# Optimization experiments

Hardware: AMD Instinct MI355X
Metric: run time of the kernel (lower is better)

## Reference

```python
import jax, jax.numpy as jnp
import numpy as np

B, TD, ND, FD, H = 16384, 256, 256, 512, 8
HID = [512, 256]


def _ln(x, g, b, eps=1e-5):
    m = jnp.mean(x, -1, keepdims=True)
    v = jnp.mean((x - m) ** 2, -1, keepdims=True)
    return (x - m) * jax.lax.rsqrt(v + eps) * g + b


def _mha1(q_in, k_in, v_in, wq, bq, wk, bk, wv, bv, wo, bo):
    # MultiheadAttention with seq_len=1 on both sides; eval mode (dropout off).
    Bq, E = q_in.shape
    dh = E // H
    q = (q_in @ wq.T + bq).reshape(Bq, H, dh)
    k = (k_in @ wk.T + bk).reshape(Bq, H, dh)
    scores = jnp.sum(q * k, -1) / np.sqrt(dh)          # [B, H]
    w = jax.nn.softmax(scores[..., None], axis=-1)      # [B, H, 1] -> exactly 1 (single key)
    attn = jnp.mean(w, axis=1)[:, None, :]              # averaged over heads -> [B, 1, 1]
    v = v_in @ wv.T + bv                                # attn weight == 1, so attn_out == v
    out = v @ wo.T + bo
    return out, attn


def setup_inputs():
    key = jax.random.key(0)
    ks = iter(jax.random.split(key, 40))
    def p(*shape):
        return jax.random.normal(next(ks), shape, dtype=jnp.float32) * 0.02
    inp = {
        'text_emb': jax.random.normal(next(ks), (B, TD), dtype=jnp.float32),
        'num_emb': jax.random.normal(next(ks), (B, ND), dtype=jnp.float32),
        'tp_w': p(FD, TD), 'tp_b': p(FD),
        'np_w': p(FD, ND), 'np_b': p(FD),
        'a1_wq': p(FD, FD), 'a1_wk': p(FD, FD), 'a1_wv': p(FD, FD),
        'a1_bq': p(FD), 'a1_bk': p(FD), 'a1_bv': p(FD),
        'a1_wo': p(FD, FD), 'a1_bo': p(FD),
        'a2_wq': p(FD, FD), 'a2_wk': p(FD, FD), 'a2_wv': p(FD, FD),
        'a2_bq': p(FD), 'a2_bk': p(FD), 'a2_bv': p(FD),
        'a2_wo': p(FD, FD), 'a2_bo': p(FD),
        'n1_g': jnp.ones((FD,), jnp.float32), 'n1_b': jnp.zeros((FD,), jnp.float32),
        'n2_g': jnp.ones((FD,), jnp.float32), 'n2_b': jnp.zeros((FD,), jnp.float32),
        'g_w': p(FD, 2 * FD), 'g_b': p(FD),
        'm1_w': p(HID[0], 2 * FD), 'm1_b': p(HID[0]),
        'ln1_g': jnp.ones((HID[0],), jnp.float32), 'ln1_b': jnp.zeros((HID[0],), jnp.float32),
        'm2_w': p(HID[1], HID[0]), 'm2_b': p(HID[1]),
        'ln2_g': jnp.ones((HID[1],), jnp.float32), 'ln2_b': jnp.zeros((HID[1],), jnp.float32),
    }
    return inp


def reference(text_emb, num_emb, tp_w, tp_b, np_w, np_b,
              a1_wq, a1_wk, a1_wv, a1_bq, a1_bk, a1_bv, a1_wo, a1_bo,
              a2_wq, a2_wk, a2_wv, a2_bq, a2_bk, a2_bv, a2_wo, a2_bo,
              n1_g, n1_b, n2_g, n2_b, g_w, g_b,
              m1_w, m1_b, ln1_g, ln1_b, m2_w, m2_b, ln2_g, ln2_b):
    t = text_emb @ tp_w.T + tp_b                        # [B, FD]
    n = num_emb @ np_w.T + np_b                         # [B, FD]
    n2t, attn_n2t = _mha1(n, t, t, a1_wq, a1_bq, a1_wk, a1_bk, a1_wv, a1_bv, a1_wo, a1_bo)
    n2t = _ln(n + n2t, n1_g, n1_b)
    t2n, attn_t2n = _mha1(t, n, n, a2_wq, a2_bq, a2_wk, a2_bk, a2_wv, a2_bv, a2_wo, a2_bo)
    t2n = _ln(t + t2n, n2_g, n2_b)
    comb = jnp.concatenate([n2t, t2n], axis=-1)         # [B, 2*FD]
    gate = jax.nn.sigmoid(comb @ g_w.T + g_b)           # [B, FD]
    h = jax.nn.gelu(_ln(comb @ m1_w.T + m1_b, ln1_g, ln1_b), approximate=False)
    fused = jax.nn.gelu(_ln(h @ m2_w.T + m2_b, ln2_g, ln2_b), approximate=False)
    return fused, gate, attn_n2t, attn_t2n
```

## Files before the change

### kernel.cpp

```cpp
#include <hip/hip_runtime.h>
#include <math.h>

typedef unsigned short u16;
typedef __bf16 bf16x8 __attribute__((ext_vector_type(8)));
typedef float f32x4 __attribute__((ext_vector_type(4)));
typedef short s16x8 __attribute__((ext_vector_type(8)));
typedef short s16x4 __attribute__((ext_vector_type(4)));

__device__ __forceinline__ float b2f(u16 u) {
    union { unsigned i; float f; } c; c.i = ((unsigned)u) << 16; return c.f;
}
__device__ __forceinline__ u16 f2b(float f) {
    union { float f; unsigned i; } c; c.f = f;
    return (u16)((c.i + 0x7fffu + ((c.i >> 16) & 1u)) >> 16);
}
__device__ __forceinline__ float gelu_f(float v) {
    return 0.5f * v * (1.0f + erff(v * 0.70710678118654752f));
}
__device__ __forceinline__ void async_cp16(const u16* g, u16* l) {
    __builtin_amdgcn_global_load_lds((const __attribute__((address_space(1))) void*)g,
                                     (__attribute__((address_space(3))) void*)l, 16, 0, 0);
}

template<int SUBN, int IR>
__global__ __launch_bounds__(256, 2)
void gemm_bt(const u16* __restrict__ A0, const u16* __restrict__ A1,
             const u16* __restrict__ W0, const u16* __restrict__ W1,
             const float* __restrict__ B0, const float* __restrict__ B1,
             const float* __restrict__ LG0, const float* __restrict__ LB0,
             const float* __restrict__ LG1, const float* __restrict__ LB1,
             void* __restrict__ O0v, void* __restrict__ O1v,
             int lda, int K, int halfBlocks, int ldo0, int ldo1,
             int mode0, int mode1)
{
    constexpr int BM   = IR * 16;
    constexpr int NCOL = 256 * SUBN;
    constexpr int WCH  = 8 * SUBN;
    constexpr int EPIW = NCOL + 8;
    constexpr int STAGEU = (BM + NCOL) * 64;
    constexpr int EPIS = (IR == 4) ? 64 * EPIW : 0;
    __shared__ u16 sm[(STAGEU > EPIS) ? STAGEU : EPIS];
    u16* sA = sm;
    u16* sW = sm + BM * 64;

    const int bx = blockIdx.x, by = blockIdx.y;
    const int half = (bx >= halfBlocks) ? 1 : 0;
    const int bxl = bx - half * halfBlocks;
    const u16* A = (half ? A1 : A0) + (size_t)by * BM * lda;
    const u16* W = (half ? W1 : W0) + (size_t)bxl * NCOL * K;
    const float* bias = half ? B1 : B0;
    const float* lng = half ? LG1 : LG0;
    const float* lnb = half ? LB1 : LB0;
    void* outv = half ? O1v : O0v;
    const int ldo = half ? ldo1 : ldo0;
    const int mode = half ? mode1 : mode0;

    const int tid = threadIdx.x;
    const int lane = tid & 63;
    const int wave = tid >> 6;
    const int fc = lane & 15;
    const int quad = lane >> 4;

    int par[2], pac[2];
#pragma unroll
    for (int c = 0; c < 2; ++c) {
        const int p = tid + 256 * c;
        par[c] = p >> 3;
        pac[c] = ((p & 7) - (par[c] & 7)) & 7;
    }
    int pwr[WCH], pwc[WCH];
#pragma unroll
    for (int c = 0; c < WCH; ++c) {
        const int p = tid + 256 * c;
        pwr[c] = p >> 3;
        pwc[c] = ((p & 7) - (pwr[c] & 7)) & 7;
    }

    f32x4 acc[IR][4 * SUBN];
#pragma unroll
    for (int i = 0; i < IR; ++i)
#pragma unroll
        for (int j = 0; j < 4 * SUBN; ++j)
            acc[i][j] = f32x4{0.f, 0.f, 0.f, 0.f};

    for (int k0 = 0; k0 < K; k0 += 64) {
#pragma unroll
        for (int c = 0; c < 2; ++c) {
            const int p = tid + 256 * c;
            if (p < BM * 8)
                async_cp16(A + (size_t)par[c] * lda + k0 + pac[c] * 8, &sA[p * 8]);
        }
#pragma unroll
        for (int c = 0; c < WCH; ++c)
            async_cp16(W + (size_t)pwr[c] * K + k0 + pwc[c] * 8,
                       &sW[(tid + 256 * c) * 8]);
        __syncthreads();

#pragma unroll
        for (int kk = 0; kk < 2; ++kk) {
            bf16x8 af[IR];
#pragma unroll
            for (int i = 0; i < IR; ++i) {
                const int ar = i * 16 + fc;
                const int slot = ar * 8 + ((kk * 4 + quad + (ar & 7)) & 7);
                af[i] = *(const bf16x8*)&sA[slot * 8];
            }
#pragma unroll
            for (int sub = 0; sub < SUBN; ++sub) {
                bf16x8 wf[4];
#pragma unroll
                for (int j = 0; j < 4; ++j) {
                    const int wr = wave * 64 * SUBN + sub * 64 + j * 16 + fc;
                    const int slot = wr * 8 + ((kk * 4 + quad + (wr & 7)) & 7);
                    wf[j] = *(const bf16x8*)&sW[slot * 8];
                }
#pragma unroll
                for (int i = 0; i < IR; ++i)
#pragma unroll
                    for (int j = 0; j < 4; ++j)
                        acc[i][sub * 4 + j] =
                            __builtin_amdgcn_mfma_f32_16x16x32_bf16(af[i], wf[j], acc[i][sub * 4 + j], 0, 0, 0);
            }
        }
        __syncthreads();
    }

    const int colb = bxl * NCOL;

    if (mode <= 1) {
#pragma unroll
        for (int sub = 0; sub < SUBN; ++sub)
#pragma unroll
        for (int j = 0; j < 4; ++j) {
            const int colh = colb + wave * 64 * SUBN + sub * 64 + j * 16 + fc;
            const float bv = bias[colh];
#pragma unroll
            for (int i = 0; i < IR; ++i)
#pragma unroll
            for (int r = 0; r < 4; ++r) {
                const int row = by * BM + i * 16 + quad * 4 + r;
                const float v = acc[i][sub * 4 + j][r] + bv;
                if (mode == 1)
                    ((float*)outv)[(size_t)row * ldo + colh] = 1.0f / (1.0f + expf(-v));
                else
                    ((u16*)outv)[(size_t)row * ldo + colh] = f2b(v);
            }
        }
    } else if constexpr (IR == 4) {
        float bb[SUBN * 4];
#pragma unroll
        for (int sub = 0; sub < SUBN; ++sub)
#pragma unroll
        for (int j = 0; j < 4; ++j)
            bb[sub * 4 + j] = bias[colb + wave * 64 * SUBN + sub * 64 + j * 16 + fc];
#pragma unroll
        for (int sub = 0; sub < SUBN; ++sub)
#pragma unroll
        for (int j = 0; j < 4; ++j) {
            const int col = wave * 64 * SUBN + sub * 64 + j * 16 + fc;
#pragma unroll
            for (int i = 0; i < 4; ++i)
#pragma unroll
            for (int r = 0; r < 4; ++r)
                sm[(i * 16 + quad * 4 + r) * EPIW + col] =
                    f2b(acc[i][sub * 4 + j][r] + bb[sub * 4 + j]);
        }
        __syncthreads();

        constexpr int CE = NCOL / 64;
        constexpr float INV = 1.0f / (float)NCOL;
        float gv[CE], bvv[CE];
#pragma unroll
        for (int e = 0; e < CE; ++e) {
            gv[e] = lng[lane * CE + e];
            bvv[e] = lnb[lane * CE + e];
        }
        for (int rr = 0; rr < 16; ++rr) {
            const int rl = wave * 16 + rr;
            const int grow = by * 64 + rl;
            float x[CE], s = 0.f, ss = 0.f;
            if constexpr (CE == 8) {
                s16x8 xv = *(const s16x8*)&sm[rl * EPIW + lane * 8];
#pragma unroll
                for (int e = 0; e < 8; ++e) { x[e] = b2f((u16)xv[e]); s += x[e]; ss += x[e] * x[e]; }
            } else {
                s16x4 xv = *(const s16x4*)&sm[rl * EPIW + lane * 4];
#pragma unroll
                for (int e = 0; e < 4; ++e) { x[e] = b2f((u16)xv[e]); s += x[e]; ss += x[e] * x[e]; }
            }
#pragma unroll
            for (int m = 32; m >= 1; m >>= 1) { s += __shfl_xor(s, m, 64); ss += __shfl_xor(ss, m, 64); }
            const float mean = s * INV;
            const float var = ss * INV - mean * mean;
            const float rs = rsqrtf(var + 1e-5f);
            float y[CE];
#pragma unroll
            for (int e = 0; e < CE; ++e) {
                y[e] = (x[e] - mean) * rs * gv[e] + bvv[e];
                if (mode >= 3) y[e] = gelu_f(y[e]);
            }
            if (mode == 4) {
                float* o = (float*)outv;
#pragma unroll
                for (int e = 0; e < CE; ++e)
                    o[(size_t)grow * ldo + colb + lane * CE + e] = y[e];
                if (lane == 0) {
                    o[(size_t)16384 * 768 + grow] = 1.0f;
                    o[(size_t)16384 * 769 + grow] = 1.0f;
                }
            } else {
                u16* o = (u16*)outv;
                if constexpr (CE == 8) {
                    s16x8 ov;
#pragma unroll
                    for (int e = 0; e < 8; ++e) ov[e] = (short)f2b(y[e]);
                    *(s16x8*)&o[(size_t)grow * ldo + colb + lane * 8] = ov;
                } else {
                    s16x4 ov;
#pragma unroll
                    for (int e = 0; e < 4; ++e) ov[e] = (short)f2b(y[e]);
                    *(s16x4*)&o[(size_t)grow * ldo + colb + lane * 4] = ov;
                }
            }
        }
    }
}


__device__ __forceinline__ void cvt_quads(const float* __restrict__ src,
                                          u16* __restrict__ dst, int bi, int tid)
{
#pragma unroll
    for (int c = 0; c < 2; ++c) {
        const int q = bi * 512 + tid + 256 * c;
        f32x4 v = *(const f32x4*)(src + (size_t)q * 4);
        s16x4 o;
        o[0] = (short)f2b(v[0]); o[1] = (short)f2b(v[1]);
        o[2] = (short)f2b(v[2]); o[3] = (short)f2b(v[3]);
        *(s16x4*)(dst + (size_t)q * 4) = o;
    }
}

__device__ void transpose_cvt64(const float* __restrict__ src, int C,
                                u16* __restrict__ dst, int R,
                                int tr, int tc, int tid, float* sm)
{
    const int lr = tid >> 4, lc4 = (tid & 15) * 4;
#pragma unroll
    for (int m = 0; m < 4; ++m) {
        const int i = lr + m * 16;
        f32x4 v = *(const f32x4*)&src[(size_t)(tr + i) * C + tc + lc4];
#pragma unroll
        for (int mm = 0; mm < 4; ++mm) sm[i * 65 + lc4 + mm] = v[mm];
    }
    __syncthreads();
#pragma unroll
    for (int m = 0; m < 4; ++m) {
        const int j = lr + m * 16;
        s16x4 o;
#pragma unroll
        for (int mm = 0; mm < 4; ++mm)
            o[mm] = (short)f2b(sm[(size_t)(lc4 + mm) * 65 + j]);
        *(s16x4*)&dst[(size_t)(tc + j) * R + tr + lc4] = o;
    }
}

__device__ void matvec_rows(const float* __restrict__ M, const float* __restrict__ v,
                            const float* __restrict__ add1, const float* __restrict__ add2,
                            float* __restrict__ out, int r0, int tid, float* sm)
{
    for (int i = tid; i < 512; i += 256) sm[i] = v[i];
    __syncthreads();
    const int row = r0 + (tid & 63), q = tid >> 6;
    float s = 0.f;
    for (int k = q * 128; k < q * 128 + 128; k += 4) {
        f32x4 m = *(const f32x4*)&M[(size_t)row * 512 + k];
        s += m[0] * sm[k] + m[1] * sm[k + 1] + m[2] * sm[k + 2] + m[3] * sm[k + 3];
    }
    sm[512 + tid] = s;
    __syncthreads();
    if (tid < 64)
        out[r0 + tid] = sm[512 + tid] + sm[512 + tid + 64] + sm[512 + tid + 128] +
                        sm[512 + tid + 192] + add1[r0 + tid] + add2[r0 + tid];
}

__global__ __launch_bounds__(256)
void prep_cvt(const float* __restrict__ text, const float* __restrict__ num,
              const float* __restrict__ tp_w, const float* __restrict__ np_w,
              const float* __restrict__ g_w, const float* __restrict__ m1_w,
              const float* __restrict__ m2_w,
              const float* __restrict__ a1_wv, const float* __restrict__ a2_wv,
              const float* __restrict__ a1_wo, const float* __restrict__ a2_wo,
              const float* __restrict__ a1_bv, const float* __restrict__ a1_bo,
              const float* __restrict__ a2_bv, const float* __restrict__ a2_bo,
              const float* __restrict__ tp_b, const float* __restrict__ np_b,
              u16* __restrict__ EMBc, u16* __restrict__ Wbig,
              u16* __restrict__ g_bf, u16* __restrict__ m1_bf, u16* __restrict__ m2_bf,
              u16* __restrict__ a1_wvT, u16* __restrict__ a2_wvT,
              u16* __restrict__ tp_wT, u16* __restrict__ np_wT,
              u16* __restrict__ a1_wo_bf, u16* __restrict__ a2_wo_bf,
              float* __restrict__ w1, float* __restrict__ w2,
              float* __restrict__ zb)
{
    __shared__ float smem[64 * 65];
    const int b = blockIdx.x, tid = threadIdx.x;
    if (b < 4096) {
#pragma unroll
        for (int c = 0; c < 2; ++c) {
            const int q = b * 512 + tid + 256 * c;
            const int e = q * 4, row = e >> 9, col = e & 511;
            const float* src = (col < 256) ? text + (size_t)row * 256 + col
                                           : num + (size_t)row * 256 + (col - 256);
            f32x4 v = *(const f32x4*)src;
            s16x4 o;
            o[0] = (short)f2b(v[0]); o[1] = (short)f2b(v[1]);
            o[2] = (short)f2b(v[2]); o[3] = (short)f2b(v[3]);
            *(s16x4*)(EMBc + e) = o;
        }
    } else if (b < 4352) { cvt_quads(g_w, g_bf, b - 4096, tid); }
    else if (b < 4608) { cvt_quads(m1_w, m1_bf, b - 4352, tid); }
    else if (b < 4672) { cvt_quads(m2_w, m2_bf, b - 4608, tid); }
    else if (b < 4736) {
#pragma unroll
        for (int c = 0; c < 2; ++c) {
            const int q = (b - 4672) * 512 + tid + 256 * c;
            const int e = q * 4, row = e >> 8, col = e & 255;
            f32x4 v = *(const f32x4*)(np_w + e);
            s16x4 o;
            o[0] = (short)f2b(v[0]); o[1] = (short)f2b(v[1]);
            o[2] = (short)f2b(v[2]); o[3] = (short)f2b(v[3]);
            *(s16x4*)(Wbig + (size_t)row * 512 + 256 + col) = o;
        }
    } else if (b < 4800) {
#pragma unroll
        for (int c = 0; c < 2; ++c) {
            const int q = (b - 4736) * 512 + tid + 256 * c;
            const int e = q * 4, row = e >> 8, col = e & 255;
            f32x4 v = *(const f32x4*)(tp_w + e);
            s16x4 o;
            o[0] = (short)f2b(v[0]); o[1] = (short)f2b(v[1]);
            o[2] = (short)f2b(v[2]); o[3] = (short)f2b(v[3]);
            *(s16x4*)(Wbig + (size_t)(512 + row) * 512 + col) = o;
        }
    } else if (b < 4864) {
        const int t = b - 4800;
        transpose_cvt64(a1_wv, 512, a1_wvT, 512, (t >> 3) * 64, (t & 7) * 64, tid, smem);
    } else if (b < 4928) {
        const int t = b - 4864;
        transpose_cvt64(a2_wv, 512, a2_wvT, 512, (t >> 3) * 64, (t & 7) * 64, tid, smem);
    } else if (b < 4960) {
        const int t = b - 4928;
        transpose_cvt64(tp_w, 256, tp_wT, 512, (t >> 2) * 64, (t & 3) * 64, tid, smem);
    } else if (b < 4992) {
        const int t = b - 4960;
        transpose_cvt64(np_w, 256, np_wT, 512, (t >> 2) * 64, (t & 3) * 64, tid, smem);
    } else if (b < 5120) { cvt_quads(a1_wo, a1_wo_bf, b - 4992, tid); }
    else if (b < 5248) { cvt_quads(a2_wo, a2_wo_bf, b - 5120, tid); }
    else if (b < 5256) {
        matvec_rows(a1_wo, a1_bv, a1_bo, np_b, w1, (b - 5248) * 64, tid, smem);
    } else if (b < 5264) {
        matvec_rows(a2_wo, a2_bv, a2_bo, tp_b, w2, (b - 5256) * 64, tid, smem);
    } else {
        *(f32x4*)&zb[tid * 4] = f32x4{0.f, 0.f, 0.f, 0.f};
    }
}

__global__ __launch_bounds__(256)
void prep_bias(const u16* __restrict__ M1, const u16* __restrict__ M2,
               const float* __restrict__ tp_b, const float* __restrict__ np_b,
               const float* __restrict__ w1, const float* __restrict__ w2,
               float* __restrict__ bbig)
{
    __shared__ float sm[768];
    const int b = blockIdx.x, tid = threadIdx.x;
    const int side = b >> 3, r0 = (b & 7) * 64;
    const u16* M = side ? M2 : M1;
    const float* v = side ? np_b : tp_b;
    const float* w = side ? w2 : w1;
    float* out = bbig + side * 512;
    for (int i = tid; i < 512; i += 256) sm[i] = v[i];
    __syncthreads();
    const int row = r0 + (tid & 63), q = tid >> 6;
    float s = 0.f;
    for (int k = q * 128; k < q * 128 + 128; k += 8) {
        s16x8 m = *(const s16x8*)&M[(size_t)row * 512 + k];
#pragma unroll
        for (int j = 0; j < 8; ++j) s += b2f((u16)m[j]) * sm[k + j];
    }
    sm[512 + tid] = s;
    __syncthreads();
    if (tid < 64)
        out[r0 + tid] = sm[512 + tid] + sm[512 + tid + 64] + sm[512 + tid + 128] +
                        sm[512 + tid + 192] + w[r0 + tid];
}

extern "C" void kernel_launch(void* const* d_in, const int* in_sizes, int n_in,
                              void* d_out, int out_size, void* d_ws, size_t ws_size,
                              hipStream_t stream)
{
    const float* text  = (const float*)d_in[0];
    const float* num   = (const float*)d_in[1];
    const float* tp_w  = (const float*)d_in[2];
    const float* tp_b  = (const float*)d_in[3];
    const float* np_w  = (const float*)d_in[4];
    const float* np_b  = (const float*)d_in[5];
    const float* a1_wv = (const float*)d_in[8];
    const float* a1_bv = (const float*)d_in[11];
    const float* a1_wo = (const float*)d_in[12];
    const float* a1_bo = (const float*)d_in[13];
    const float* a2_wv = (const float*)d_in[16];
    const float* a2_bv = (const float*)d_in[19];
    const float* a2_wo = (const float*)d_in[20];
    const float* a2_bo = (const float*)d_in[21];
    const float* n1_g  = (const float*)d_in[22];
    const float* n1_b  = (const float*)d_in[23];
    const float* n2_g  = (const float*)d_in[24];
    const float* n2_b  = (const float*)d_in[25];
    const float* g_w   = (const float*)d_in[26];
    const float* g_b   = (const float*)d_in[27];
    const float* m1_w  = (const float*)d_in[28];
    const float* m1_b  = (const float*)d_in[29];
    const float* ln1_g = (const float*)d_in[30];
    const float* ln1_b = (const float*)d_in[31];
    const float* m2_w  = (const float*)d_in[32];
    const float* m2_b  = (const float*)d_in[33];
    const float* ln2_g = (const float*)d_in[34];
    const float* ln2_b = (const float*)d_in[35];

    float* outp = (float*)d_out;
    char* ob = (char*)d_out;
    char* ws = (char*)d_ws;
    const size_t KB = 1024, MB = 1048576;

    u16* Wbig    = (u16*)(ob);
    u16* g_bf    = (u16*)(ob + 1 * MB);
    u16* m1_bf   = (u16*)(ob + 2 * MB);
    u16* a1_wvT  = (u16*)(ob + 3 * MB + 256 * KB);
    u16* a2_wvT  = (u16*)(ob + 3 * MB + 768 * KB);
    u16* tp_wT   = (u16*)(ob + 4 * MB + 256 * KB);
    u16* np_wT   = (u16*)(ob + 4 * MB + 512 * KB);
    u16* a1_wo_bf= (u16*)(ob + 4 * MB + 768 * KB);
    u16* a2_wo_bf= (u16*)(ob + 5 * MB + 256 * KB);
    u16* M1      = (u16*)(ob + 5 * MB + 768 * KB);
    u16* M2      = (u16*)(ob + 6 * MB + 256 * KB);
    float* w1    = (float*)(ob + 6 * MB + 768 * KB);
    float* w2    = w1 + 512;
    float* bbig  = w1 + 1024;
    float* zb    = w1 + 2048;
    u16* EMBc    = (u16*)(ob + 16 * MB);
    u16* X     = (u16*)ws;
    u16* m2_bf = (u16*)(ws + 32 * MB);
    u16* h     = (u16*)(ws + 48 * MB);

    dim3 blk(256);

    prep_cvt<<<5265, blk, 0, stream>>>(text, num, tp_w, np_w, g_w, m1_w, m2_w,
        a1_wv, a2_wv, a1_wo, a2_wo, a1_bv, a1_bo, a2_bv, a2_bo, tp_b, np_b,
        EMBc, Wbig, g_bf, m1_bf, m2_bf, a1_wvT, a2_wvT, tp_wT, np_wT,
        a1_wo_bf, a2_wo_bf, w1, w2, zb);
    gemm_bt<1, 1><<<dim3(4, 32), blk, 0, stream>>>(a1_wo_bf, a2_wo_bf, a1_wvT, a2_wvT,
        zb, zb, nullptr, nullptr, nullptr, nullptr,
        M1, M2, 512, 512, 2, 512, 512, 0, 0);
    prep_bias<<<16, blk, 0, stream>>>(M1, M2, tp_b, np_b, w1, w2, bbig);
    gemm_bt<1, 1><<<dim3(2, 32), blk, 0, stream>>>(M1, M2, tp_wT, np_wT,
        zb, zb, nullptr, nullptr, nullptr, nullptr,
        Wbig, Wbig + (size_t)512 * 512 + 256, 512, 512, 1, 512, 512, 0, 0);
    gemm_bt<2, 4><<<dim3(2, 256), blk, 0, stream>>>(EMBc, EMBc,
        Wbig, Wbig + (size_t)512 * 512, bbig, bbig + 512,
        n1_g, n1_b, n2_g, n2_b,
        X, X + 512, 512, 512, 1, 1024, 1024, 2, 2);
    gemm_bt<2, 4><<<dim3(2, 256), blk, 0, stream>>>(X, X, g_bf, m1_bf, g_b, m1_b,
        nullptr, nullptr, ln1_g, ln1_b,
        outp + (size_t)16384 * 256, h, 1024, 1024, 1, 512, 512, 1, 3);
    gemm_bt<1, 4><<<dim3(1, 256), blk, 0, stream>>>(h, h, m2_bf, m2_bf, m2_b, m2_b,
        ln2_g, ln2_b, ln2_g, ln2_b,
        outp, outp, 512, 512, 1, 256, 256, 4, 4);
}
```

Baseline: 299.7 us.

## Add 512-thread 128x512 tile GEMM kernel for the two large projections

Introduces a new gemm_big kernel with 8 waves per block, each block computing a 128-row by 512-column tile with a 2x4 wave grid and 4x8 MFMA fragments per wave, and uses it for the fused projection and gate/MLP1 GEMMs in place of the templated 64-row kernel. The larger tile raises operand reuse per LDS load and halves the number of blocks, while the sigmoid and layernorm/GELU epilogues are reimplemented through shared-memory staging. The K loop is single-buffered with no prefetch overlap, and the large accumulator array increases register pressure, which may limit occupancy.

```diff
diff --git a/kernel.cpp b/kernel.cpp
--- a/kernel.cpp
+++ b/kernel.cpp
@@ -20,6 +20,179 @@
 __device__ __forceinline__ void async_cp16(const u16* g, u16* l) {
     __builtin_amdgcn_global_load_lds((const __attribute__((address_space(1))) void*)g,
                                      (__attribute__((address_space(3))) void*)l, 16, 0, 0);
+}
+
+__global__ __launch_bounds__(512, 2)
+void gemm_big(const u16* __restrict__ A0, const u16* __restrict__ A1,
+              const u16* __restrict__ W0, const u16* __restrict__ W1,
+              const float* __restrict__ B0, const float* __restrict__ B1,
+              const float* __restrict__ LG0, const float* __restrict__ LB0,
+              const float* __restrict__ LG1, const float* __restrict__ LB1,
+              void* __restrict__ O0v, void* __restrict__ O1v,
+              int lda, int K, int ldo0, int ldo1, int mode0, int mode1)
+{
+    __shared__ u16 sm[(128 + 512) * 64];
+    u16* sA = sm;
+    u16* sW = sm + 128 * 64;
+
+    const int half = blockIdx.x;
+    const int by = blockIdx.y;
+    const u16* A = (half ? A1 : A0) + (size_t)by * 128 * lda;
+    const u16* W = half ? W1 : W0;
+    const float* bias = half ? B1 : B0;
+    const float* lng = half ? LG1 : LG0;
+    const float* lnb = half ? LB1 : LB0;
+    void* outv = half ? O1v : O0v;
+    const int ldo = half ? ldo1 : ldo0;
+    const int mode = half ? mode1 : mode0;
+
+    const int tid = threadIdx.x;
+    const int lane = tid & 63;
+    const int wave = tid >> 6;
+    const int wrow = wave >> 2;
+    const int wcol = wave & 3;
+    const int fc = lane & 15;
+    const int quad = lane >> 4;
+
+    int par[2], pac[2];
+#pragma unroll
+    for (int c = 0; c < 2; ++c) {
+        const int p = tid + 512 * c;
+        par[c] = p >> 3;
+        pac[c] = ((p & 7) - (par[c] & 7)) & 7;
+    }
+    int pwr[8], pwc[8];
+#pragma unroll
+    for (int c = 0; c < 8; ++c) {
+        const int p = tid + 512 * c;
+        pwr[c] = p >> 3;
+        pwc[c] = ((p & 7) - (pwr[c] & 7)) & 7;
+    }
+
+    f32x4 acc[4][8];
+#pragma unroll
+    for (int i = 0; i < 4; ++i)
+#pragma unroll
+        for (int j = 0; j < 8; ++j)
+            acc[i][j] = f32x4{0.f, 0.f, 0.f, 0.f};
+
+    for (int k0 = 0; k0 < K; k0 += 64) {
+#pragma unroll
+        for (int c = 0; c < 2; ++c)
+            async_cp16(A + (size_t)par[c] * lda + k0 + pac[c] * 8, &sA[(tid + 512 * c) * 8]);
+#pragma unroll
+        for (int c = 0; c < 8; ++c)
+            async_cp16(W + (size_t)pwr[c] * K + k0 + pwc[c] * 8, &sW[(tid + 512 * c) * 8]);
+        __syncthreads();
+
+#pragma unroll
+        for (int kk = 0; kk < 2; ++kk) {
+            bf16x8 af[4];
+#pragma unroll
+            for (int i = 0; i < 4; ++i) {
+                const int ar = wrow * 64 + i * 16 + fc;
+                const int slot = ar * 8 + ((kk * 4 + quad + (ar & 7)) & 7);
+                af[i] = *(const bf16x8*)&sA[slot * 8];
+            }
+            bf16x8 wf[8];
+#pragma unroll
+            for (int j = 0; j < 8; ++j) {
+                const int wr = wcol * 128 + j * 16 + fc;
+                const int slot = wr * 8 + ((kk * 4 + quad + (wr & 7)) & 7);
+                wf[j] = *(const bf16x8*)&sW[slot * 8];
+            }
+#pragma unroll
+            for (int i = 0; i < 4; ++i)
+#pragma unroll
+            for (int j = 0; j < 8; ++j)
+                acc[i][j] =
+                    __builtin_amdgcn_mfma_f32_16x16x32_bf16(af[i], wf[j], acc[i][j], 0, 0, 0);
+        }
+        __syncthreads();
+    }
+
+    float bb[8];
+#pragma unroll
+    for (int j = 0; j < 8; ++j)
+        bb[j] = bias[wcol * 128 + j * 16 + fc];
+
+    if (mode == 1) {
+        float* smf = (float*)sm;
+#pragma unroll
+        for (int p = 0; p < 4; ++p) {
+            if (wrow == (p >> 1)) {
+#pragma unroll
+                for (int i2 = 0; i2 < 2; ++i2) {
+                    const int i = 2 * (p & 1) + i2;
+#pragma unroll
+                    for (int j = 0; j < 8; ++j) {
+                        const int col = wcol * 128 + j * 16 + fc;
+#pragma unroll
+                        for (int r = 0; r < 4; ++r) {
+                            const int lr = i2 * 16 + quad * 4 + r;
+                            smf[lr * 516 + col] =
+                                1.0f / (1.0f + expf(-(acc[i][j][r] + bb[j])));
+                        }
+                    }
+                }
+            }
+            __syncthreads();
+            const int rl = tid >> 4, c0 = (tid & 15) * 32;
+            const int grow = by * 128 + p * 32 + rl;
+            float* o = (float*)outv;
+#pragma unroll
+            for (int k = 0; k < 8; ++k)
+                *(f32x4*)&o[(size_t)grow * ldo + c0 + 4 * k] =
+                    *(const f32x4*)&smf[rl * 516 + c0 + 4 * k];
+            __syncthreads();
+        }
+    } else {
+        float gv[8], bvv[8];
+#pragma unroll
+        for (int e = 0; e < 8; ++e) {
+            gv[e] = lng[lane * 8 + e];
+            bvv[e] = lnb[lane * 8 + e];
+        }
+#pragma unroll
+        for (int p = 0; p < 2; ++p) {
+            if (wrow == p) {
+#pragma unroll
+                for (int i = 0; i < 4; ++i)
+#pragma unroll
+                for (int j = 0; j < 8; ++j) {
+                    const int col = wcol * 128 + j * 16 + fc;
+#pragma unroll
+                    for (int r = 0; r < 4; ++r) {
+                        const int lr = i * 16 + quad * 4 + r;
+                        sm[lr * 520 + col] = f2b(acc[i][j][r] + bb[j]);
+                    }
+                }
+            }
+            __syncthreads();
+            for (int rr = 0; rr < 8; ++rr) {
+                const int rl = wave * 8 + rr;
+                const int grow = by * 128 + p * 64 + rl;
+                float x[8], s = 0.f, ss = 0.f;
+                s16x8 xv = *(const s16x8*)&sm[rl * 520 + lane * 8];
+#pragma unroll
+                for (int e = 0; e < 8; ++e) { x[e] = b2f((u16)xv[e]); s += x[e]; ss += x[e] * x[e]; }
+#pragma unroll
+                for (int m = 32; m >= 1; m >>= 1) { s += __shfl_xor(s, m, 64); ss += __shfl_xor(ss, m, 64); }
+                const float mean = s * (1.f / 512.f);
+                const float var = ss * (1.f / 512.f) - mean * mean;
+                const float rs = rsqrtf(var + 1e-5f);
+                s16x8 ov;
+#pragma unroll
+                for (int e = 0; e < 8; ++e) {
+                    float y = (x[e] - mean) * rs * gv[e] + bvv[e];
+                    if (mode == 3) y = gelu_f(y);
+                    ov[e] = (short)f2b(y);
+                }
+                *(s16x8*)&((u16*)outv)[(size_t)grow * ldo + lane * 8] = ov;
+            }
+            __syncthreads();
+        }
+    }
 }
 
 template<int SUBN, int IR>
@@ -465,13 +638,13 @@
     gemm_bt<1, 1><<<dim3(2, 32), blk, 0, stream>>>(M1, M2, tp_wT, np_wT,
         zb, zb, nullptr, nullptr, nullptr, nullptr,
         Wbig, Wbig + (size_t)512 * 512 + 256, 512, 512, 1, 512, 512, 0, 0);
-    gemm_bt<2, 4><<<dim3(2, 256), blk, 0, stream>>>(EMBc, EMBc,
+    gemm_big<<<dim3(2, 128), dim3(512), 0, stream>>>(EMBc, EMBc,
         Wbig, Wbig + (size_t)512 * 512, bbig, bbig + 512,
         n1_g, n1_b, n2_g, n2_b,
-        X, X + 512, 512, 512, 1, 1024, 1024, 2, 2);
-    gemm_bt<2, 4><<<dim3(2, 256), blk, 0, stream>>>(X, X, g_bf, m1_bf, g_b, m1_b,
+        X, X + 512, 512, 512, 1024, 1024, 2, 2);
+    gemm_big<<<dim3(2, 128), dim3(512), 0, stream>>>(X, X, g_bf, m1_bf, g_b, m1_b,
         nullptr, nullptr, ln1_g, ln1_b,
-        outp + (size_t)16384 * 256, h, 1024, 1024, 1, 512, 512, 1, 3);
+        outp + (size_t)16384 * 256, h, 1024, 1024, 512, 512, 1, 3);
     gemm_bt<1, 4><<<dim3(1, 256), blk, 0, stream>>>(h, h, m2_bf, m2_bf, m2_b, m2_b,
         ln2_g, ln2_b, ln2_g, ln2_b,
         outp, outp, 512, 512, 1, 256, 256, 4, 4);
```

Result: slower. 315.9 us (+5.4%).

## Load weight fragments directly from global into registers and double-buffer A tiles

Applied to the files above, without the earlier changes.

Adds a REGW template path for the two large fused GEMMs. Weight fragments are read straight from global memory (L2-resident) into registers instead of being staged through LDS, and the activation tile is double-buffered in LDS with the next tile's async copy issued before compute. The sigmoid gate epilogue also goes through LDS so the fp32 output is written with coalesced vector stores. This removes the large per-iteration W staging and one barrier, but adds per-wave global load latency on the MFMA critical path and redundant W reads across row blocks.

```diff
diff --git a/kernel.cpp b/kernel.cpp
--- a/kernel.cpp
+++ b/kernel.cpp
@@ -22,7 +22,7 @@
                                      (__attribute__((address_space(3))) void*)l, 16, 0, 0);
 }
 
-template<int SUBN, int IR>
+template<int SUBN, int IR, int REGW>
 __global__ __launch_bounds__(256, 2)
 void gemm_bt(const u16* __restrict__ A0, const u16* __restrict__ A1,
              const u16* __restrict__ W0, const u16* __restrict__ W1,
@@ -37,7 +37,7 @@
     constexpr int NCOL = 256 * SUBN;
     constexpr int WCH  = 8 * SUBN;
     constexpr int EPIW = NCOL + 8;
-    constexpr int STAGEU = (BM + NCOL) * 64;
+    constexpr int STAGEU = REGW ? 2 * BM * 64 : (BM + NCOL) * 64;
     constexpr int EPIS = (IR == 4) ? 64 * EPIW : 0;
     __shared__ u16 sm[(STAGEU > EPIS) ? STAGEU : EPIS];
     u16* sA = sm;
@@ -68,13 +68,6 @@
         par[c] = p >> 3;
         pac[c] = ((p & 7) - (par[c] & 7)) & 7;
     }
-    int pwr[WCH], pwc[WCH];
-#pragma unroll
-    for (int c = 0; c < WCH; ++c) {
-        const int p = tid + 256 * c;
-        pwr[c] = p >> 3;
-        pwc[c] = ((p & 7) - (pwr[c] & 7)) & 7;
-    }
 
     f32x4 acc[IR][4 * SUBN];
 #pragma unroll
@@ -83,67 +76,156 @@
         for (int j = 0; j < 4 * SUBN; ++j)
             acc[i][j] = f32x4{0.f, 0.f, 0.f, 0.f};
 
-    for (int k0 = 0; k0 < K; k0 += 64) {
-#pragma unroll
-        for (int c = 0; c < 2; ++c) {
+    if constexpr (REGW) {
+        auto STAGE_A = [&](int buf, int k0) {
+#pragma unroll
+            for (int c = 0; c < 2; ++c) {
+                const int p = tid + 256 * c;
+                if (p < BM * 8)
+                    async_cp16(A + (size_t)par[c] * lda + k0 + pac[c] * 8,
+                               &sm[buf * (BM * 64) + p * 8]);
+            }
+        };
+        STAGE_A(0, 0);
+        __syncthreads();
+        int buf = 0;
+        const int NT = K >> 6;
+        for (int t = 0; t < NT; ++t) {
+            const int k0 = t << 6;
+            if (t + 1 < NT) STAGE_A(buf ^ 1, (t + 1) << 6);
+            const u16* sAb = sm + buf * (BM * 64);
+#pragma unroll
+            for (int kk = 0; kk < 2; ++kk) {
+                bf16x8 af[IR];
+#pragma unroll
+                for (int i = 0; i < IR; ++i) {
+                    const int ar = i * 16 + fc;
+                    const int slot = ar * 8 + ((kk * 4 + quad + (ar & 7)) & 7);
+                    af[i] = *(const bf16x8*)&sAb[slot * 8];
+                }
+#pragma unroll
+                for (int sub = 0; sub < SUBN; ++sub) {
+                    bf16x8 wf[4];
+#pragma unroll
+                    for (int j = 0; j < 4; ++j) {
+                        const int wr = wave * 64 * SUBN + sub * 64 + j * 16 + fc;
+                        wf[j] = *(const bf16x8*)(W + (size_t)wr * K + k0 + kk * 32 + quad * 8);
+                    }
+#pragma unroll
+                    for (int i = 0; i < IR; ++i)
+#pragma unroll
+                        for (int j = 0; j < 4; ++j)
+                            acc[i][sub * 4 + j] =
+                                __builtin_amdgcn_mfma_f32_16x16x32_bf16(af[i], wf[j], acc[i][sub * 4 + j], 0, 0, 0);
+                }
+            }
+            __syncthreads();
+            buf ^= 1;
+        }
+    } else {
+        int pwr[WCH], pwc[WCH];
+#pragma unroll
+        for (int c = 0; c < WCH; ++c) {
             const int p = tid + 256 * c;
-            if (p < BM * 8)
-                async_cp16(A + (size_t)par[c] * lda + k0 + pac[c] * 8, &sA[p * 8]);
-        }
-#pragma unroll
-        for (int c = 0; c < WCH; ++c)
-            async_cp16(W + (size_t)pwr[c] * K + k0 + pwc[c] * 8,
-                       &sW[(tid + 256 * c) * 8]);
-        __syncthreads();
-
-#pragma unroll
-        for (int kk = 0; kk < 2; ++kk) {
-            bf16x8 af[IR];
-#pragma unroll
-            for (int i = 0; i < IR; ++i) {
-                const int ar = i * 16 + fc;
-                const int slot = ar * 8 + ((kk * 4 + quad + (ar & 7)) & 7);
-                af[i] = *(const bf16x8*)&sA[slot * 8];
-            }
-#pragma unroll
-            for (int sub = 0; sub < SUBN; ++sub) {
-                bf16x8 wf[4];
+            pwr[c] = p >> 3;
+            pwc[c] = ((p & 7) - (pwr[c] & 7)) & 7;
+        }
+        for (int k0 = 0; k0 < K; k0 += 64) {
+#pragma unroll
+            for (int c = 0; c < 2; ++c) {
+                const int p = tid + 256 * c;
+                if (p < BM * 8)
+                    async_cp16(A + (size_t)par[c] * lda + k0 + pac[c] * 8, &sA[p * 8]);
+            }
+#pragma unroll
+            for (int c = 0; c < WCH; ++c)
+                async_cp16(W + (size_t)pwr[c] * K + k0 + pwc[c] * 8,
+                           &sW[(tid + 256 * c) * 8]);
+            __syncthreads();
+
+#pragma unroll
+            for (int kk = 0; kk < 2; ++kk) {
+                bf16x8 af[IR];
+#pragma unroll
+                for (int i = 0; i < IR; ++i) {
+                    const int ar = i * 16 + fc;
+                    const int slot = ar * 8 + ((kk * 4 + quad + (ar & 7)) & 7);
+                    af[i] = *(const bf16x8*)&sA[slot * 8];
+                }
+#pragma unroll
+                for (int sub = 0; sub < SUBN; ++sub) {
+                    bf16x8 wf[4];
+#pragma unroll
+                    for (int j = 0; j < 4; ++j) {
+                        const int wr = wave * 64 * SUBN + sub * 64 + j * 16 + fc;
+                        const int slot = wr * 8 + ((kk * 4 + quad + (wr & 7)) & 7);
+                        wf[j] = *(const bf16x8*)&sW[slot * 8];
+                    }
+#pragma unroll
+                    for (int i = 0; i < IR; ++i)
+#pragma unroll
+                        for (int j = 0; j < 4; ++j)
+                            acc[i][sub * 4 + j] =
+                                __builtin_amdgcn_mfma_f32_16x16x32_bf16(af[i], wf[j], acc[i][sub * 4 + j], 0, 0, 0);
+                }
+            }
+            __syncthreads();
+        }
+    }
+
+    const int colb = bxl * NCOL;
+
+    if (mode <= 1) {
+        if constexpr (REGW) {
+            float* sf = (float*)sm;
+            float bb2[SUBN * 4];
+#pragma unroll
+            for (int sub = 0; sub < SUBN; ++sub)
+#pragma unroll
+            for (int j = 0; j < 4; ++j)
+                bb2[sub * 4 + j] = bias[colb + wave * 64 * SUBN + sub * 64 + j * 16 + fc];
+#pragma unroll
+            for (int q = 0; q < IR; ++q) {
+#pragma unroll
+                for (int sub = 0; sub < SUBN; ++sub)
 #pragma unroll
                 for (int j = 0; j < 4; ++j) {
-                    const int wr = wave * 64 * SUBN + sub * 64 + j * 16 + fc;
-                    const int slot = wr * 8 + ((kk * 4 + quad + (wr & 7)) & 7);
-                    wf[j] = *(const bf16x8*)&sW[slot * 8];
-                }
+                    const int col = wave * 64 * SUBN + sub * 64 + j * 16 + fc;
+#pragma unroll
+                    for (int r = 0; r < 4; ++r)
+                        sf[(quad * 4 + r) * 516 + col] =
+                            1.0f / (1.0f + expf(-(acc[q][sub * 4 + j][r] + bb2[sub * 4 + j])));
+                }
+                __syncthreads();
+                float* o = (float*)outv;
+#pragma unroll
+                for (int it = 0; it < 8; ++it) {
+                    const int rl = it * 2 + (tid >> 7);
+                    const int cidx = (tid & 127) * 4;
+                    const int grow = by * BM + q * 16 + rl;
+                    *(f32x4*)&o[(size_t)grow * ldo + colb + cidx] =
+                        *(const f32x4*)&sf[rl * 516 + cidx];
+                }
+                __syncthreads();
+            }
+        } else {
+#pragma unroll
+            for (int sub = 0; sub < SUBN; ++sub)
+#pragma unroll
+            for (int j = 0; j < 4; ++j) {
+                const int colh = colb + wave * 64 * SUBN + sub * 64 + j * 16 + fc;
+                const float bv = bias[colh];
 #pragma unroll
                 for (int i = 0; i < IR; ++i)
 #pragma unroll
-                    for (int j = 0; j < 4; ++j)
-                        acc[i][sub * 4 + j] =
-                            __builtin_amdgcn_mfma_f32_16x16x32_bf16(af[i], wf[j], acc[i][sub * 4 + j], 0, 0, 0);
-            }
-        }
-        __syncthreads();
-    }
-
-    const int colb = bxl * NCOL;
-
-    if (mode <= 1) {
-#pragma unroll
-        for (int sub = 0; sub < SUBN; ++sub)
-#pragma unroll
-        for (int j = 0; j < 4; ++j) {
-            const int colh = colb + wave * 64 * SUBN + sub * 64 + j * 16 + fc;
-            const float bv = bias[colh];
-#pragma unroll
-            for (int i = 0; i < IR; ++i)
-#pragma unroll
-            for (int r = 0; r < 4; ++r) {
-                const int row = by * BM + i * 16 + quad * 4 + r;
-                const float v = acc[i][sub * 4 + j][r] + bv;
-                if (mode == 1)
-                    ((float*)outv)[(size_t)row * ldo + colh] = 1.0f / (1.0f + expf(-v));
-                else
-                    ((u16*)outv)[(size_t)row * ldo + colh] = f2b(v);
+                for (int r = 0; r < 4; ++r) {
+                    const int row = by * BM + i * 16 + quad * 4 + r;
+                    const float v = acc[i][sub * 4 + j][r] + bv;
+                    if (mode == 1)
+                        ((float*)outv)[(size_t)row * ldo + colh] = 1.0f / (1.0f + expf(-v));
+                    else
+                        ((u16*)outv)[(size_t)row * ldo + colh] = f2b(v);
+                }
             }
         }
     } else if constexpr (IR == 4) {
@@ -458,21 +540,21 @@
         a1_wv, a2_wv, a1_wo, a2_wo, a1_bv, a1_bo, a2_bv, a2_bo, tp_b, np_b,
         EMBc, Wbig, g_bf, m1_bf, m2_bf, a1_wvT, a2_wvT, tp_wT, np_wT,
         a1_wo_bf, a2_wo_bf, w1, w2, zb);
-    gemm_bt<1, 1><<<dim3(4, 32), blk, 0, stream>>>(a1_wo_bf, a2_wo_bf, a1_wvT, a2_wvT,
+    gemm_bt<1, 1, 0><<<dim3(4, 32), blk, 0, stream>>>(a1_wo_bf, a2_wo_bf, a1_wvT, a2_wvT,
         zb, zb, nullptr, nullptr, nullptr, nullptr,
         M1, M2, 512, 512, 2, 512, 512, 0, 0);
     prep_bias<<<16, blk, 0, stream>>>(M1, M2, tp_b, np_b, w1, w2, bbig);
-    gemm_bt<1, 1><<<dim3(2, 32), blk, 0, stream>>>(M1, M2, tp_wT, np_wT,
+    gemm_bt<1, 1, 0><<<dim3(2, 32), blk, 0, stream>>>(M1, M2, tp_wT, np_wT,
         zb, zb, nullptr, nullptr, nullptr, nullptr,
         Wbig, Wbig + (size_t)512 * 512 + 256, 512, 512, 1, 512, 512, 0, 0);
-    gemm_bt<2, 4><<<dim3(2, 256), blk, 0, stream>>>(EMBc, EMBc,
+    gemm_bt<2, 4, 1><<<dim3(2, 256), blk, 0, stream>>>(EMBc, EMBc,
         Wbig, Wbig + (size_t)512 * 512, bbig, bbig + 512,
         n1_g, n1_b, n2_g, n2_b,
         X, X + 512, 512, 512, 1, 1024, 1024, 2, 2);
-    gemm_bt<2, 4><<<dim3(2, 256), blk, 0, stream>>>(X, X, g_bf, m1_bf, g_b, m1_b,
+    gemm_bt<2, 4, 1><<<dim3(2, 256), blk, 0, stream>>>(X, X, g_bf, m1_bf, g_b, m1_b,
         nullptr, nullptr, ln1_g, ln1_b,
         outp + (size_t)16384 * 256, h, 1024, 1024, 1, 512, 512, 1, 3);
-    gemm_bt<1, 4><<<dim3(1, 256), blk, 0, stream>>>(h, h, m2_bf, m2_bf, m2_b, m2_b,
+    gemm_bt<1, 4, 0><<<dim3(1, 256), blk, 0, stream>>>(h, h, m2_bf, m2_bf, m2_b, m2_b,
         ln2_g, ln2_b, ln2_g, ln2_b,
         outp, outp, 512, 512, 1, 256, 256, 4, 4);
 }
```

Result: slower. 346.9 us (+15.7%).
